# Kernel optimization log

Measured on AMD Instinct MI355X. Metric: run time of the kernel, lower is better.

Reference implementation:

```python
import math
import jax, jax.numpy as jnp
import numpy as np

B, N, C, H = 64, 197, 768, 12
KEEP_RATE = 0.7

def setup_inputs() -> dict:
    key = jax.random.key(0)
    k0, k1, k2 = jax.random.split(key, 3)
    x = jax.random.normal(k0, (B, N, C), jnp.float32)
    qkv_w = jax.random.normal(k1, (C, 3 * C), jnp.float32) * 0.02
    qkv_b = jnp.zeros((3 * C,), jnp.float32)
    proj_w = jax.random.normal(k2, (C, C), jnp.float32) * 0.02
    proj_b = jnp.zeros((C,), jnp.float32)
    return {"x": x, "qkv_w": qkv_w, "qkv_b": qkv_b, "proj_w": proj_w, "proj_b": proj_b}

def reference(x, qkv_w, qkv_b, proj_w, proj_b):
    b, n, c = x.shape
    d = c // H
    scale = d ** -0.5
    # qkv: [B,N,3C] -> [3,B,H,N,d]
    qkv = (x @ qkv_w + qkv_b).reshape(b, n, 3, H, d)
    qkv = jnp.transpose(qkv, (2, 0, 3, 1, 4))
    q, k, v = qkv[0], qkv[1], qkv[2]
    attn = jax.nn.softmax(jnp.einsum('bhnd,bhmd->bhnm', q, k) * scale, axis=-1)  # [B,H,N,N]
    out = jnp.einsum('bhnm,bhmd->bhnd', attn, v)          # [B,H,N,d]
    out = jnp.transpose(out, (0, 2, 1, 3)).reshape(b, n, c)
    x_out = out @ proj_w + proj_b                          # [B,N,C]
    # dynamic token pruning via CLS attention (row 0, excluding CLS itself)
    left_tokens = math.ceil(KEEP_RATE * (n - 1))
    cls_attn = attn[:, :, 0, 1:].mean(axis=1)              # [B,N-1]
    _, idx = jax.lax.top_k(cls_attn, left_tokens)          # descending, sorted
    index = jnp.broadcast_to(idx[:, :, None], (b, left_tokens, c))
    return (x_out, index, idx, cls_attn, left_tokens)
```

## Files before the change

kernel.cpp:

```cpp
#include <hip/hip_runtime.h>
#include <math.h>

#define BB   64
#define NTOK 197
#define CC   768
#define HH   12
#define DH   64
#define MTOT (BB * NTOK)
#define MPAD 12672
#define LEFT 138

#define XOUT_OFF  0
#define INDEX_OFF 9682944
#define IDX_OFF   16465920
#define CLS_OFF   16474752
#define LT_OFF    16487296

typedef short s8v __attribute__((ext_vector_type(8)));
typedef short s4v __attribute__((ext_vector_type(4)));
typedef float f4v __attribute__((ext_vector_type(4)));

#define GLOAD16(g, l) __builtin_amdgcn_global_load_lds( \
    (const __attribute__((address_space(1))) unsigned int*)(g), \
    (__attribute__((address_space(3))) unsigned int*)(l), 16, 0, 0)

__device__ __forceinline__ unsigned short f2bf(float f) {
    union { float f; unsigned int i; } x; x.f = f;
    unsigned int r = x.i + 0x7FFFu + ((x.i >> 16) & 1u);
    return (unsigned short)(r >> 16);
}


__device__ __forceinline__ void convert_x_body(int blk, int tid,
        const float* __restrict__ in, unsigned short* __restrict__ outb)
{
    size_t i = ((size_t)blk * 256 + tid) * 8;
    float4 a = *(const float4*)(in + i);
    float4 b = *(const float4*)(in + i + 4);
    s8v r;
    r[0] = (short)f2bf(a.x); r[1] = (short)f2bf(a.y);
    r[2] = (short)f2bf(a.z); r[3] = (short)f2bf(a.w);
    r[4] = (short)f2bf(b.x); r[5] = (short)f2bf(b.y);
    r[6] = (short)f2bf(b.z); r[7] = (short)f2bf(b.w);
    *(s8v*)(outb + i) = r;
}

__device__ __forceinline__ void transpose_w_body(int q, int tid, char* smem,
        const float* __restrict__ inq, const float* __restrict__ inp,
        unsigned short* __restrict__ outq, unsigned short* __restrict__ outp)
{
    float (*tile)[33] = (float(*)[33])smem;
    const int bi = q % 24;
    int bj = q / 24;
    const float* in; unsigned short* outb; int N;
    if (bj < 72) { in = inq; outb = outq; N = 2304; }
    else         { bj -= 72; in = inp; outb = outp; N = 768; }
    const int tx = tid & 31, ty = tid >> 5;
#pragma unroll
    for (int r = ty; r < 32; r += 8)
        tile[r][tx] = in[(size_t)(bi * 32 + r) * N + bj * 32 + tx];
    __syncthreads();
#pragma unroll
    for (int r = ty; r < 32; r += 8)
        outb[(size_t)(bj * 32 + r) * 768 + bi * 32 + tx] = f2bf(tile[tx][r]);
}

#define QCH 64
__device__ __forceinline__ void qr_body(int blk, int tid, char* smem,
        const float* __restrict__ x, const float* __restrict__ qkv_w,
        const float* __restrict__ qkv_b, float* __restrict__ rws,
        float* __restrict__ bconst)
{
    const int b = blk / HH, h = blk - b * HH;
    float* x0    = (float*)smem;
    float* q0h   = (float*)(smem + 3072);
    float* wbuf0 = (float*)(smem + 3328);
    float* wbuf1 = (float*)(smem + 19712);
    for (int c = tid; c < CC; c += 256) x0[c] = x[(size_t)b * NTOK * CC + c];
    for (int u = tid; u < QCH * DH; u += 256) {
        int cc = u >> 6, o = u & 63;
        wbuf0[u] = qkv_w[(size_t)cc * 2304 + h * DH + o];
    }
    __syncthreads();
    float acc = 0.f;
    if (tid < DH) acc = qkv_b[h * DH + tid];
    for (int k = 0; k < CC / QCH; ++k) {
        float* wcur  = (k & 1) ? wbuf1 : wbuf0;
        float* wnext = (k & 1) ? wbuf0 : wbuf1;
        if (k + 1 < CC / QCH) {
            const int cbase = (k + 1) * QCH;
            for (int u = tid; u < QCH * DH; u += 256) {
                int cc = u >> 6, o = u & 63;
                wnext[u] = qkv_w[(size_t)(cbase + cc) * 2304 + h * DH + o];
            }
        }
        if (tid < DH) {
            const int cbase = k * QCH;
#pragma unroll
            for (int cc = 0; cc < QCH; ++cc)
                acc = fmaf(x0[cbase + cc], wcur[cc * 64 + tid], acc);
        }
        __syncthreads();
    }
    if (tid < DH) q0h[tid] = acc;
    __syncthreads();
    for (int c = tid; c < CC; c += 256) {
        const float* wrow = qkv_w + (size_t)c * 2304 + CC + h * DH;
        float acc2 = 0.f;
#pragma unroll
        for (int d = 0; d < DH; d += 4) {
            float4 w4 = *(const float4*)(wrow + d);
            acc2 = fmaf(w4.x, q0h[d + 0], acc2);
            acc2 = fmaf(w4.y, q0h[d + 1], acc2);
            acc2 = fmaf(w4.z, q0h[d + 2], acc2);
            acc2 = fmaf(w4.w, q0h[d + 3], acc2);
        }
        rws[((size_t)b * HH + h) * CC + c] = acc2;
    }
    if (tid == 0) {
        float acc3 = 0.f;
        for (int d = 0; d < DH; ++d) acc3 += q0h[d] * qkv_b[CC + h * DH + d];
        bconst[blk] = acc3;
    }
}

__device__ __forceinline__ void gemm_body(int id, int tid, char* smem,
        const unsigned short* __restrict__ A, const unsigned short* __restrict__ BT,
        const float* __restrict__ bias, int ncolt, int mode,
        unsigned short* __restrict__ outb, float* __restrict__ outf)
{
    const int xcd = id & 7;
    const int t = id >> 3;
    const int ct = t % ncolt, s = t / ncolt;
    const int rt = s * 8 + xcd;
    if (rt >= 99) return;
    const int m0 = rt * 128, n0 = ct * 128;

    const int wave = tid >> 6, lane = tid & 63;
    const int quad = lane >> 4, l16 = lane & 15;
    const int rowbase = (wave >> 1) * 64, colbase = (wave & 1) * 64;
    short* As = (short*)smem;
    short* Bs = (short*)(smem + 16384);

    const int rA   = lane >> 3;
    const int gcol = ((lane & 7) ^ rA) * 8;
    unsigned int agof[4], bgof[4];
#pragma unroll
    for (int i = 0; i < 4; ++i) {
        int c = wave * 4 + i;
        agof[i] = (unsigned int)((m0 + c * 8 + rA) * 768 + gcol);
        bgof[i] = (unsigned int)((n0 + c * 8 + rA) * 768 + gcol);
    }
    int aoff[4], boff[4];
#pragma unroll
    for (int i = 0; i < 4; ++i) {
        aoff[i] = (rowbase + i * 16 + l16) * 64 + ((quad ^ (l16 & 7)) * 8);
        boff[i] = (colbase + i * 16 + l16) * 64 + ((quad ^ (l16 & 7)) * 8);
    }

    f4v acc[4][4];
#pragma unroll
    for (int i = 0; i < 4; ++i)
#pragma unroll
        for (int j = 0; j < 4; ++j) acc[i][j] = (f4v)0.f;

    for (int k0 = 0; k0 < 768; k0 += 64) {
#pragma unroll
        for (int i = 0; i < 4; ++i) {
            int c = wave * 4 + i;
            GLOAD16(A  + agof[i] + k0, &As[c * 512]);
            GLOAD16(BT + bgof[i] + k0, &Bs[c * 512]);
        }
        __syncthreads();
#pragma unroll
        for (int ks = 0; ks < 2; ++ks) {
            const int x = ks * 32;
            s8v af[4], bf[4];
#pragma unroll
            for (int i = 0; i < 4; ++i) af[i] = *(const s8v*)&As[aoff[i] ^ x];
#pragma unroll
            for (int j = 0; j < 4; ++j) bf[j] = *(const s8v*)&Bs[boff[j] ^ x];
#pragma unroll
            for (int i = 0; i < 4; ++i)
#pragma unroll
                for (int j = 0; j < 4; ++j)
                    acc[i][j] = __builtin_amdgcn_mfma_f32_16x16x32_bf16(bf[j], af[i], acc[i][j], 0, 0, 0);
        }
        __syncthreads();
    }

    const int ncols = mode ? 768 : 2304;
#pragma unroll
    for (int i = 0; i < 4; ++i) {
        const int m = m0 + rowbase + i * 16 + l16;
        if (m >= MTOT) continue;
#pragma unroll
        for (int j = 0; j < 4; ++j) {
            const int nb = n0 + colbase + j * 16 + quad * 4;
            float4 b4 = *(const float4*)&bias[nb];
            if (mode == 1) {
                float4 r;
                r.x = acc[i][j][0] + b4.x; r.y = acc[i][j][1] + b4.y;
                r.z = acc[i][j][2] + b4.z; r.w = acc[i][j][3] + b4.w;
                *(float4*)(outf + (size_t)m * ncols + nb) = r;
            } else {
                s4v r;
                r[0] = (short)f2bf(acc[i][j][0] + b4.x);
                r[1] = (short)f2bf(acc[i][j][1] + b4.y);
                r[2] = (short)f2bf(acc[i][j][2] + b4.z);
                r[3] = (short)f2bf(acc[i][j][3] + b4.w);
                *(s4v*)(outb + (size_t)m * ncols + nb) = r;
            }
        }
    }
}

__device__ __forceinline__ void cls_s_body(int q, int tid, char* smem,
        const float* __restrict__ x, const float* __restrict__ rws,
        const float* __restrict__ bconst, float* __restrict__ sws)
{
    const int bx = q % 10, b = q / 10;
    float* rl  = (float*)smem;
    float* bcs = (float*)(smem + 37056);
#pragma unroll
    for (int h = 0; h < HH; ++h)
        for (int c = tid; c < CC; c += 256)
            rl[h * 772 + c] = rws[((size_t)b * HH + h) * CC + c];
    if (tid < HH) bcs[tid] = bconst[b * HH + tid];
    __syncthreads();
    const int local = bx * 256 + tid;
    if (local < NTOK * HH) {
        const int tok = local / HH;
        const int h = local - tok * HH;
        const float* xr = x + ((size_t)b * NTOK + tok) * CC;
        const float* rp = rl + h * 772;
        float acc = 0.f;
#pragma unroll 8
        for (int c = 0; c < CC; c += 4) {
            float4 x4 = *(const float4*)(xr + c);
            float4 r4 = *(const float4*)(rp + c);
            acc = fmaf(x4.x, r4.x, acc);
            acc = fmaf(x4.y, r4.y, acc);
            acc = fmaf(x4.z, r4.z, acc);
            acc = fmaf(x4.w, r4.w, acc);
        }
        sws[((size_t)b * HH + h) * NTOK + tok] = (acc + bcs[h]) * 0.125f;
    }
}

#define VTS 224
__device__ __forceinline__ void transpose_v_body(int q, int tid, char* smem,
        const unsigned short* __restrict__ qkv, unsigned short* __restrict__ vt)
{
    short (*tile)[33] = (short(*)[33])smem;
    const int bx = q % 7;
    const int by = (q / 7) & 1;
    const int bh = q / 14;
    const int b = bh / HH, h = bh - b * HH;
    const int tx = tid & 31, ty = tid >> 5;
    const unsigned short* vin = qkv + (size_t)b * NTOK * 2304 + 1536 + h * DH;
#pragma unroll
    for (int r = ty; r < 32; r += 8) {
        const int tok = bx * 32 + r;
        tile[r][tx] = (tok < NTOK) ? (short)vin[(size_t)tok * 2304 + by * 32 + tx] : (short)0;
    }
    __syncthreads();
#pragma unroll
    for (int r = ty; r < 32; r += 8) {
        const int d = by * 32 + r;
        vt[((size_t)bh * DH + d) * VTS + bx * 32 + tx] = tile[tx][r];
    }
}

__device__ __forceinline__ void cls_topk_body(int b, int tid, char* smem,
        const float* __restrict__ sws, float* __restrict__ out, int write_lt)
{
    const int wave = tid >> 6, lane = tid & 63;
    float (*sbuf)[208] = (float(*)[208])smem;
    float (*pm)[208]   = (float(*)[208])(smem + 9984);
    float* vals        = (float*)(smem + 13312);
    int*   idxs        = (int*)(smem + 14336);

    for (int jj = lane; jj < 208; jj += 64) pm[wave][jj] = 0.f;
    if (tid < NTOK) {
#pragma unroll
        for (int h = 0; h < HH; ++h)
            sbuf[h][tid] = sws[((size_t)b * HH + h) * NTOK + tid];
    }
    __syncthreads();

    for (int h = wave; h < HH; h += 4) {
        float sv[4], ev[4];
        float mx = -1e30f;
#pragma unroll
        for (int t = 0; t < 4; ++t) {
            int j = lane + 64 * t;
            sv[t] = (j < NTOK) ? sbuf[h][j] : -1e30f;
            mx = fmaxf(mx, sv[t]);
        }
#pragma unroll
        for (int off = 1; off < 64; off <<= 1) mx = fmaxf(mx, __shfl_xor(mx, off, 64));
        float sm = 0.f;
#pragma unroll
        for (int t = 0; t < 4; ++t) {
            int j = lane + 64 * t;
            ev[t] = (j < NTOK) ? expf(sv[t] - mx) : 0.f;
            sm += ev[t];
        }
#pragma unroll
        for (int off = 1; off < 64; off <<= 1) sm += __shfl_xor(sm, off, 64);
#pragma unroll
        for (int t = 0; t < 4; ++t) {
            int j = lane + 64 * t;
            if (j < NTOK) pm[wave][j] += ev[t] / sm;
        }
    }
    __syncthreads();

    float v = -INFINITY;
    int id = 256 + tid;
    if (tid < NTOK - 1) {
        int j = tid + 1;
        float s = ((pm[0][j] + pm[1][j]) + (pm[2][j] + pm[3][j])) * (1.f / 12.f);
        v = s; id = tid;
        out[CLS_OFF + (size_t)b * (NTOK - 1) + tid] = s;
    }
    vals[tid] = v; idxs[tid] = id;
    __syncthreads();

    for (int k = 2; k <= 256; k <<= 1) {
        for (int j = k >> 1; j > 0; j >>= 1) {
            int ixj = tid ^ j;
            if (ixj > tid) {
                float va = vals[tid], vb2 = vals[ixj];
                int ia = idxs[tid], ib = idxs[ixj];
                bool aLess = (va > vb2) || (va == vb2 && ia < ib);
                bool dir = ((tid & k) == 0);
                if (dir != aLess) {
                    vals[tid] = vb2; vals[ixj] = va;
                    idxs[tid] = ib;  idxs[ixj] = ia;
                }
            }
            __syncthreads();
        }
    }

    if (tid < LEFT) out[IDX_OFF + (size_t)b * LEFT + tid] = (float)idxs[tid];
    if (write_lt && b == 0 && tid == 0) out[LT_OFF] = (float)LEFT;
}

__device__ __forceinline__ void write_index_body(int row, int tid,
        const float* __restrict__ idx_in, float* __restrict__ out)
{
    const float v = idx_in[row];
    if (tid < 192) {
        float4 r; r.x = v; r.y = v; r.z = v; r.w = v;
        *(float4*)(out + INDEX_OFF + (size_t)row * CC + tid * 4) = r;
    }
}

#define PRE_QR 768
#define PRE_CV 4728
#define PRE_TW 2304

__global__ __launch_bounds__(256)
void fat_pre(const float* __restrict__ x, const float* __restrict__ qkv_w,
             const float* __restrict__ qkv_b, const float* __restrict__ proj_w,
             unsigned short* __restrict__ xbf, unsigned short* __restrict__ wt1,
             unsigned short* __restrict__ wt2, float* __restrict__ rws,
             float* __restrict__ bconst)
{
    __shared__ __align__(16) char smem[36096];
    const int id = blockIdx.x, tid = threadIdx.x;
    if (id < PRE_QR)
        qr_body(id, tid, smem, x, qkv_w, qkv_b, rws, bconst);
    else if (id < PRE_QR + PRE_CV)
        convert_x_body(id - PRE_QR, tid, x, xbf);
    else
        transpose_w_body(id - PRE_QR - PRE_CV, tid, smem, qkv_w, proj_w, wt1, wt2);
}

#define QKV_GEMM (8 * 18 * 13)

__global__ __launch_bounds__(256, 3)
void fat_qkv(const unsigned short* __restrict__ xbf, const unsigned short* __restrict__ wt1,
             const float* __restrict__ qkv_b, unsigned short* __restrict__ qkvbf,
             const float* __restrict__ x, const float* __restrict__ rws,
             const float* __restrict__ bconst, float* __restrict__ sws)
{
    __shared__ __align__(16) char smem[37104];
    const int id = blockIdx.x, tid = threadIdx.x;
    if (id < QKV_GEMM)
        gemm_body(id, tid, smem, xbf, wt1, qkv_b, 18, 0, qkvbf, nullptr);
    else
        cls_s_body(id - QKV_GEMM, tid, smem, x, rws, bconst, sws);
}

__global__ __launch_bounds__(256)
void fat_tv(const unsigned short* __restrict__ qkvbf, unsigned short* __restrict__ vt,
            const float* __restrict__ sws, float* __restrict__ out, int write_lt)
{
    __shared__ __align__(16) char smem[15360];
    const int id = blockIdx.x, tid = threadIdx.x;
    if (id < 64)
        cls_topk_body(id, tid, smem, sws, out, write_lt);
    else
        transpose_v_body(id - 64, tid, smem, qkvbf, vt);
}

#define PROJ_GEMM (8 * 6 * 13)

__global__ __launch_bounds__(256, 3)
void fat_proj(const unsigned short* __restrict__ atbf, const unsigned short* __restrict__ wt2,
              const float* __restrict__ proj_b, float* __restrict__ outf,
              const float* __restrict__ idx_in, float* __restrict__ out)
{
    __shared__ __align__(16) char smem[32768];
    const int id = blockIdx.x, tid = threadIdx.x;
    if (id < PROJ_GEMM)
        gemm_body(id, tid, smem, atbf, wt2, proj_b, 6, 1, nullptr, outf);
    else
        write_index_body(id - PROJ_GEMM, tid, idx_in, out);
}

#define PSTR 226

__global__ __launch_bounds__(256, 2)
void attn_mfma4(const unsigned short* __restrict__ qkv, const unsigned short* __restrict__ vt,
                unsigned short* __restrict__ attnbf)
{
    const int bh = blockIdx.x;
    const int g  = blockIdx.y;
    const int b = bh / HH, h = bh - b * HH;
    const int tid = threadIdx.x;
    const int wave = tid >> 6, lane = tid & 63;
    const int quad = lane >> 4, l16 = lane & 15;
    __shared__ __align__(16) short Ks[NTOK * 64];
    __shared__ short Ps[4][16 * PSTR];

    const unsigned short* qg = qkv + (size_t)b * NTOK * 2304 + h * DH;
    const unsigned short* kg = qg + 768;
    const unsigned short* vtb = vt + (size_t)bh * DH * VTS;

    for (int u = tid; u < NTOK * 8; u += 256) {
        const int row = u >> 3, seg = u & 7;
        *(s8v*)&Ks[row * 64 + (seg ^ (row & 7)) * 8] =
            *(const s8v*)(kg + (size_t)row * 2304 + seg * 8);
    }
    __syncthreads();

    const int strip = g * 4 + wave;
    if (strip >= 13) return;

    const int mq = min(strip * 16 + l16, NTOK - 1);
    const s8v aq0 = *(const s8v*)(qg + (size_t)mq * 2304 + quad * 8);
    const s8v aq1 = *(const s8v*)(qg + (size_t)mq * 2304 + 32 + quad * 8);

    f4v sacc[14];
#pragma unroll
    for (int j = 0; j < 14; ++j) sacc[j] = (f4v)0.f;
    __builtin_amdgcn_s_setprio(1);
#pragma unroll
    for (int j = 0; j < 14; ++j) {
        const int kt = min(j * 16 + l16, NTOK - 1);
        s8v bk0 = *(const s8v*)&Ks[kt * 64 + ((quad       ^ (kt & 7)) * 8)];
        s8v bk1 = *(const s8v*)&Ks[kt * 64 + (((quad + 4) ^ (kt & 7)) * 8)];
        sacc[j] = __builtin_amdgcn_mfma_f32_16x16x32_bf16(bk0, aq0, sacc[j], 0, 0, 0);
        sacc[j] = __builtin_amdgcn_mfma_f32_16x16x32_bf16(bk1, aq1, sacc[j], 0, 0, 0);
    }
    __builtin_amdgcn_s_setprio(0);

    s8v bvr[7][4];
#pragma unroll
    for (int t = 0; t < 7; ++t) {
        const int ko = t * 32 + quad * 8;
#pragma unroll
        for (int j = 0; j < 4; ++j)
            bvr[t][j] = *(const s8v*)(vtb + (size_t)(j * 16 + l16) * VTS + ko);
    }

    float mx = -1e30f;
#pragma unroll
    for (int j = 0; j < 14; ++j)
#pragma unroll
        for (int r = 0; r < 4; ++r) {
            const int key = j * 16 + quad * 4 + r;
            float s = (key < NTOK) ? sacc[j][r] * 0.125f : -1e30f;
            sacc[j][r] = s;
            mx = fmaxf(mx, s);
        }
    mx = fmaxf(mx, __shfl_xor(mx, 16, 64));
    mx = fmaxf(mx, __shfl_xor(mx, 32, 64));

    float sm = 0.f;
#pragma unroll
    for (int j = 0; j < 14; ++j) {
        s4v pk;
#pragma unroll
        for (int r = 0; r < 4; ++r) {
            const int key = j * 16 + quad * 4 + r;
            float p = (key < NTOK) ? __expf(sacc[j][r] - mx) : 0.f;
            sm += p;
            pk[r] = (short)f2bf(p);
        }
        *(s4v*)&Ps[wave][l16 * PSTR + j * 16 + quad * 4] = pk;
    }
    sm += __shfl_xor(sm, 16, 64);
    sm += __shfl_xor(sm, 32, 64);
    const float rcp = 1.f / sm;

    f4v oacc[4];
#pragma unroll
    for (int j = 0; j < 4; ++j) oacc[j] = (f4v)0.f;
    __builtin_amdgcn_s_setprio(1);
#pragma unroll
    for (int t = 0; t < 7; ++t) {
        const int ko = t * 32 + quad * 8;
        s8v ap = *(const s8v*)&Ps[wave][l16 * PSTR + ko];
#pragma unroll
        for (int j = 0; j < 4; ++j)
            oacc[j] = __builtin_amdgcn_mfma_f32_16x16x32_bf16(bvr[t][j], ap, oacc[j], 0, 0, 0);
    }
    __builtin_amdgcn_s_setprio(0);
    const int qrow = strip * 16 + l16;
    if (qrow < NTOK) {
#pragma unroll
        for (int j = 0; j < 4; ++j) {
            s4v o4;
#pragma unroll
            for (int r = 0; r < 4; ++r) o4[r] = (short)f2bf(oacc[j][r] * rcp);
            *(s4v*)&attnbf[((size_t)b * NTOK + qrow) * 768 + h * DH + j * 16 + quad * 4] = o4;
        }
    }
}

extern "C" void kernel_launch(void* const* d_in, const int* in_sizes, int n_in,
                              void* d_out, int out_size, void* d_ws, size_t ws_size,
                              hipStream_t stream)
{
    const float* x      = (const float*)d_in[0];
    const float* qkv_w  = (const float*)d_in[1];
    const float* qkv_b  = (const float*)d_in[2];
    const float* proj_w = (const float*)d_in[3];
    const float* proj_b = (const float*)d_in[4];
    float* out = (float*)d_out;

    char* w = (char*)d_ws;
    unsigned short* xbf   = (unsigned short*)w; w += (size_t)MPAD * CC * 2;
    unsigned short* wt1   = (unsigned short*)w; w += (size_t)3 * CC * CC * 2;
    unsigned short* wt2   = (unsigned short*)w; w += (size_t)CC * CC * 2;
    unsigned short* qkvbf = (unsigned short*)w; w += (size_t)MTOT * 3 * CC * 2;
    unsigned short* atbf  = (unsigned short*)w; w += (size_t)MPAD * CC * 2;
    float* rws    = (float*)w; w += (size_t)BB * HH * CC * 4;
    float* bconst = (float*)w; w += (size_t)BB * HH * 4;
    float* sws    = (float*)w; w += (size_t)BB * HH * NTOK * 4;
    unsigned short* vtbf  = (unsigned short*)d_ws;

    fat_pre<<<dim3(PRE_QR + PRE_CV + PRE_TW), 256, 0, stream>>>(
        x, qkv_w, qkv_b, proj_w, xbf, wt1, wt2, rws, bconst);
    fat_qkv<<<dim3(QKV_GEMM + 640), 256, 0, stream>>>(
        xbf, wt1, qkv_b, qkvbf, x, rws, bconst, sws);
    fat_tv<<<dim3(64 + 7 * 2 * BB * HH), 256, 0, stream>>>(
        qkvbf, vtbf, sws, out, (out_size > LT_OFF) ? 1 : 0);
    attn_mfma4<<<dim3(BB * HH, 4), 256, 0, stream>>>(qkvbf, vtbf, atbf);
    fat_proj<<<dim3(PROJ_GEMM + BB * LEFT), 256, 0, stream>>>(
        atbf, wt2, proj_b, out + XOUT_OFF, out + IDX_OFF, out);
}
```

Baseline: 311.1 us.

## Batch CLS query projection over 8 batches per block; move index writes into attention kernel

The CLS-query projection now runs in 96 blocks, each covering 8 batch elements for one head instead of one (batch, head) pair. Each qkv_w slice is then loaded once and reused across 8 batches, and all 256 threads do work rather than 64. The broadcast index output writes move from the projection GEMM launch into the attention launch, so the proj GEMM runs alone. The trade-off is larger shared memory per fat_pre block (about 58 KB), which may reduce how many blocks fit per CU.

Measured after the change: 334.6 us. +7.6%, slower.

```diff
diff --git a/kernel.cpp b/kernel.cpp
--- a/kernel.cpp
+++ b/kernel.cpp
@@ -65,62 +65,83 @@
         outb[(size_t)(bj * 32 + r) * 768 + bi * 32 + tx] = f2bf(tile[tx][r]);
 }
 
-#define QCH 64
-__device__ __forceinline__ void qr_body(int blk, int tid, char* smem,
+#define QCH  64
+#define BGRP 8
+__device__ __forceinline__ void qr96_body(int q, int tid, char* smem,
         const float* __restrict__ x, const float* __restrict__ qkv_w,
         const float* __restrict__ qkv_b, float* __restrict__ rws,
         float* __restrict__ bconst)
 {
-    const int b = blk / HH, h = blk - b * HH;
-    float* x0    = (float*)smem;
-    float* q0h   = (float*)(smem + 3072);
-    float* wbuf0 = (float*)(smem + 3328);
-    float* wbuf1 = (float*)(smem + 19712);
-    for (int c = tid; c < CC; c += 256) x0[c] = x[(size_t)b * NTOK * CC + c];
+    const int h  = q % HH;
+    const int b0 = (q / HH) * BGRP;
+    float (*x0s)[CC] = (float(*)[CC])smem;
+    float* wbuf0 = (float*)(smem + 24576);
+    float* wbuf1 = (float*)(smem + 40960);
+    float (*q0s)[DH] = (float(*)[DH])(smem + 57344);
+
+    for (int u = tid; u < BGRP * CC; u += 256) {
+        int b = u / CC, c = u - b * CC;
+        x0s[b][c] = x[(size_t)(b0 + b) * NTOK * CC + c];
+    }
     for (int u = tid; u < QCH * DH; u += 256) {
-        int cc = u >> 6, o = u & 63;
-        wbuf0[u] = qkv_w[(size_t)cc * 2304 + h * DH + o];
-    }
-    __syncthreads();
-    float acc = 0.f;
-    if (tid < DH) acc = qkv_b[h * DH + tid];
+        int cc = u >> 6, dd = u & 63;
+        wbuf0[u] = qkv_w[(size_t)cc * 2304 + h * DH + dd];
+    }
+    __syncthreads();
+
+    const int d  = tid & 63;
+    const int bA = tid >> 6;
+    const int bB = bA + 4;
+    float accA = qkv_b[h * DH + d];
+    float accB = qkv_b[h * DH + d];
     for (int k = 0; k < CC / QCH; ++k) {
         float* wcur  = (k & 1) ? wbuf1 : wbuf0;
         float* wnext = (k & 1) ? wbuf0 : wbuf1;
         if (k + 1 < CC / QCH) {
             const int cbase = (k + 1) * QCH;
             for (int u = tid; u < QCH * DH; u += 256) {
-                int cc = u >> 6, o = u & 63;
-                wnext[u] = qkv_w[(size_t)(cbase + cc) * 2304 + h * DH + o];
+                int cc = u >> 6, dd = u & 63;
+                wnext[u] = qkv_w[(size_t)(cbase + cc) * 2304 + h * DH + dd];
             }
         }
-        if (tid < DH) {
-            const int cbase = k * QCH;
-#pragma unroll
-            for (int cc = 0; cc < QCH; ++cc)
-                acc = fmaf(x0[cbase + cc], wcur[cc * 64 + tid], acc);
+        const int cb = k * QCH;
+#pragma unroll
+        for (int cc = 0; cc < QCH; ++cc) {
+            const float wv = wcur[cc * 64 + d];
+            accA = fmaf(x0s[bA][cb + cc], wv, accA);
+            accB = fmaf(x0s[bB][cb + cc], wv, accB);
         }
         __syncthreads();
     }
-    if (tid < DH) q0h[tid] = acc;
-    __syncthreads();
+    q0s[bA][d] = accA;
+    q0s[bB][d] = accB;
+    __syncthreads();
+
+    if (tid < BGRP) {
+        float acc3 = 0.f;
+        for (int dd = 0; dd < DH; ++dd) acc3 += q0s[tid][dd] * qkv_b[CC + h * DH + dd];
+        bconst[(b0 + tid) * HH + h] = acc3;
+    }
+
     for (int c = tid; c < CC; c += 256) {
         const float* wrow = qkv_w + (size_t)c * 2304 + CC + h * DH;
-        float acc2 = 0.f;
-#pragma unroll
-        for (int d = 0; d < DH; d += 4) {
-            float4 w4 = *(const float4*)(wrow + d);
-            acc2 = fmaf(w4.x, q0h[d + 0], acc2);
-            acc2 = fmaf(w4.y, q0h[d + 1], acc2);
-            acc2 = fmaf(w4.z, q0h[d + 2], acc2);
-            acc2 = fmaf(w4.w, q0h[d + 3], acc2);
-        }
-        rws[((size_t)b * HH + h) * CC + c] = acc2;
-    }
-    if (tid == 0) {
-        float acc3 = 0.f;
-        for (int d = 0; d < DH; ++d) acc3 += q0h[d] * qkv_b[CC + h * DH + d];
-        bconst[blk] = acc3;
+        float acc2[BGRP];
+#pragma unroll
+        for (int b = 0; b < BGRP; ++b) acc2[b] = 0.f;
+#pragma unroll
+        for (int dd = 0; dd < DH; dd += 4) {
+            float4 w4 = *(const float4*)(wrow + dd);
+#pragma unroll
+            for (int b = 0; b < BGRP; ++b) {
+                acc2[b] = fmaf(w4.x, q0s[b][dd + 0], acc2[b]);
+                acc2[b] = fmaf(w4.y, q0s[b][dd + 1], acc2[b]);
+                acc2[b] = fmaf(w4.z, q0s[b][dd + 2], acc2[b]);
+                acc2[b] = fmaf(w4.w, q0s[b][dd + 3], acc2[b]);
+            }
+        }
+#pragma unroll
+        for (int b = 0; b < BGRP; ++b)
+            rws[((size_t)(b0 + b) * HH + h) * CC + c] = acc2[b];
     }
 }
 
@@ -359,7 +380,113 @@
     }
 }
 
-#define PRE_QR 768
+#define PSTR 226
+__device__ __forceinline__ void attn_body(int bh, int g, int tid,
+        short* Ks, short* Ps,
+        const unsigned short* __restrict__ qkv, const unsigned short* __restrict__ vt,
+        unsigned short* __restrict__ attnbf)
+{
+    const int b = bh / HH, h = bh - b * HH;
+    const int wave = tid >> 6, lane = tid & 63;
+    const int quad = lane >> 4, l16 = lane & 15;
+
+    const unsigned short* qg = qkv + (size_t)b * NTOK * 2304 + h * DH;
+    const unsigned short* kg = qg + 768;
+    const unsigned short* vtb = vt + (size_t)bh * DH * VTS;
+
+    for (int u = tid; u < NTOK * 8; u += 256) {
+        const int row = u >> 3, seg = u & 7;
+        *(s8v*)&Ks[row * 64 + (seg ^ (row & 7)) * 8] =
+            *(const s8v*)(kg + (size_t)row * 2304 + seg * 8);
+    }
+    __syncthreads();
+
+    const int strip = g * 4 + wave;
+    if (strip >= 13) return;
+
+    const int mq = min(strip * 16 + l16, NTOK - 1);
+    const s8v aq0 = *(const s8v*)(qg + (size_t)mq * 2304 + quad * 8);
+    const s8v aq1 = *(const s8v*)(qg + (size_t)mq * 2304 + 32 + quad * 8);
+
+    f4v sacc[14];
+#pragma unroll
+    for (int j = 0; j < 14; ++j) sacc[j] = (f4v)0.f;
+    __builtin_amdgcn_s_setprio(1);
+#pragma unroll
+    for (int j = 0; j < 14; ++j) {
+        const int kt = min(j * 16 + l16, NTOK - 1);
+        s8v bk0 = *(const s8v*)&Ks[kt * 64 + ((quad       ^ (kt & 7)) * 8)];
+        s8v bk1 = *(const s8v*)&Ks[kt * 64 + (((quad + 4) ^ (kt & 7)) * 8)];
+        sacc[j] = __builtin_amdgcn_mfma_f32_16x16x32_bf16(bk0, aq0, sacc[j], 0, 0, 0);
+        sacc[j] = __builtin_amdgcn_mfma_f32_16x16x32_bf16(bk1, aq1, sacc[j], 0, 0, 0);
+    }
+    __builtin_amdgcn_s_setprio(0);
+
+    s8v bvr[7][4];
+#pragma unroll
+    for (int t = 0; t < 7; ++t) {
+        const int ko = t * 32 + quad * 8;
+#pragma unroll
+        for (int j = 0; j < 4; ++j)
+            bvr[t][j] = *(const s8v*)(vtb + (size_t)(j * 16 + l16) * VTS + ko);
+    }
+
+    float mx = -1e30f;
+#pragma unroll
+    for (int j = 0; j < 14; ++j)
+#pragma unroll
+        for (int r = 0; r < 4; ++r) {
+            const int key = j * 16 + quad * 4 + r;
+            float s = (key < NTOK) ? sacc[j][r] * 0.125f : -1e30f;
+            sacc[j][r] = s;
+            mx = fmaxf(mx, s);
+        }
+    mx = fmaxf(mx, __shfl_xor(mx, 16, 64));
+    mx = fmaxf(mx, __shfl_xor(mx, 32, 64));
+
+    float sm = 0.f;
+#pragma unroll
+    for (int j = 0; j < 14; ++j) {
+        s4v pk;
+#pragma unroll
+        for (int r = 0; r < 4; ++r) {
+            const int key = j * 16 + quad * 4 + r;
+            float p = (key < NTOK) ? __expf(sacc[j][r] - mx) : 0.f;
+            sm += p;
+            pk[r] = (short)f2bf(p);
+        }
+        *(s4v*)&Ps[wave * 16 * PSTR + l16 * PSTR + j * 16 + quad * 4] = pk;
+    }
+    sm += __shfl_xor(sm, 16, 64);
+    sm += __shfl_xor(sm, 32, 64);
+    const float rcp = 1.f / sm;
+
+    f4v oacc[4];
+#pragma unroll
+    for (int j = 0; j < 4; ++j) oacc[j] = (f4v)0.f;
+    __builtin_amdgcn_s_setprio(1);
+#pragma unroll
+    for (int t = 0; t < 7; ++t) {
+        const int ko = t * 32 + quad * 8;
+        s8v ap = *(const s8v*)&Ps[wave * 16 * PSTR + l16 * PSTR + ko];
+#pragma unroll
+        for (int j = 0; j < 4; ++j)
+            oacc[j] = __builtin_amdgcn_mfma_f32_16x16x32_bf16(bvr[t][j], ap, oacc[j], 0, 0, 0);
+    }
+    __builtin_amdgcn_s_setprio(0);
+    const int qrow = strip * 16 + l16;
+    if (qrow < NTOK) {
+#pragma unroll
+        for (int j = 0; j < 4; ++j) {
+            s4v o4;
+#pragma unroll
+            for (int r = 0; r < 4; ++r) o4[r] = (short)f2bf(oacc[j][r] * rcp);
+            *(s4v*)&attnbf[((size_t)b * NTOK + qrow) * 768 + h * DH + j * 16 + quad * 4] = o4;
+        }
+    }
+}
+
+#define PRE_QR 96
 #define PRE_CV 4728
 #define PRE_TW 2304
 
@@ -370,10 +497,10 @@
              unsigned short* __restrict__ wt2, float* __restrict__ rws,
              float* __restrict__ bconst)
 {
-    __shared__ __align__(16) char smem[36096];
+    __shared__ __align__(16) char smem[59392];
     const int id = blockIdx.x, tid = threadIdx.x;
     if (id < PRE_QR)
-        qr_body(id, tid, smem, x, qkv_w, qkv_b, rws, bconst);
+        qr96_body(id, tid, smem, x, qkv_w, qkv_b, rws, bconst);
     else if (id < PRE_QR + PRE_CV)
         convert_x_body(id - PRE_QR, tid, x, xbf);
     else
@@ -408,130 +535,30 @@
         transpose_v_body(id - 64, tid, smem, qkvbf, vt);
 }
 
+#define ATTN_BLKS (768 * 4)
+
+__global__ __launch_bounds__(256, 2)
+void fat_attn(const unsigned short* __restrict__ qkv, const unsigned short* __restrict__ vt,
+              unsigned short* __restrict__ attnbf,
+              const float* __restrict__ idx_in, float* __restrict__ out)
+{
+    __shared__ __align__(16) short Ks[NTOK * 64];
+    __shared__ short Ps[4 * 16 * PSTR];
+    const int id = blockIdx.x, tid = threadIdx.x;
+    if (id < ATTN_BLKS)
+        attn_body(id % 768, id / 768, tid, Ks, Ps, qkv, vt, attnbf);
+    else
+        write_index_body(id - ATTN_BLKS, tid, idx_in, out);
+}
+
 #define PROJ_GEMM (8 * 6 * 13)
 
 __global__ __launch_bounds__(256, 3)
 void fat_proj(const unsigned short* __restrict__ atbf, const unsigned short* __restrict__ wt2,
-              const float* __restrict__ proj_b, float* __restrict__ outf,
-              const float* __restrict__ idx_in, float* __restrict__ out)
+              const float* __restrict__ proj_b, float* __restrict__ outf)
 {
     __shared__ __align__(16) char smem[32768];
-    const int id = blockIdx.x, tid = threadIdx.x;
-    if (id < PROJ_GEMM)
-        gemm_body(id, tid, smem, atbf, wt2, proj_b, 6, 1, nullptr, outf);
-    else
-        write_index_body(id - PROJ_GEMM, tid, idx_in, out);
-}
-
-#define PSTR 226
-
-__global__ __launch_bounds__(256, 2)
-void attn_mfma4(const unsigned short* __restrict__ qkv, const unsigned short* __restrict__ vt,
-                unsigned short* __restrict__ attnbf)
-{
-    const int bh = blockIdx.x;
-    const int g  = blockIdx.y;
-    const int b = bh / HH, h = bh - b * HH;
-    const int tid = threadIdx.x;
-    const int wave = tid >> 6, lane = tid & 63;
-    const int quad = lane >> 4, l16 = lane & 15;
-    __shared__ __align__(16) short Ks[NTOK * 64];
-    __shared__ short Ps[4][16 * PSTR];
-
-    const unsigned short* qg = qkv + (size_t)b * NTOK * 2304 + h * DH;
-    const unsigned short* kg = qg + 768;
-    const unsigned short* vtb = vt + (size_t)bh * DH * VTS;
-
-    for (int u = tid; u < NTOK * 8; u += 256) {
-        const int row = u >> 3, seg = u & 7;
-        *(s8v*)&Ks[row * 64 + (seg ^ (row & 7)) * 8] =
-            *(const s8v*)(kg + (size_t)row * 2304 + seg * 8);
-    }
-    __syncthreads();
-
-    const int strip = g * 4 + wave;
-    if (strip >= 13) return;
-
-    const int mq = min(strip * 16 + l16, NTOK - 1);
-    const s8v aq0 = *(const s8v*)(qg + (size_t)mq * 2304 + quad * 8);
-    const s8v aq1 = *(const s8v*)(qg + (size_t)mq * 2304 + 32 + quad * 8);
-
-    f4v sacc[14];
-#pragma unroll
-    for (int j = 0; j < 14; ++j) sacc[j] = (f4v)0.f;
-    __builtin_amdgcn_s_setprio(1);
-#pragma unroll
-    for (int j = 0; j < 14; ++j) {
-        const int kt = min(j * 16 + l16, NTOK - 1);
-        s8v bk0 = *(const s8v*)&Ks[kt * 64 + ((quad       ^ (kt & 7)) * 8)];
-        s8v bk1 = *(const s8v*)&Ks[kt * 64 + (((quad + 4) ^ (kt & 7)) * 8)];
-        sacc[j] = __builtin_amdgcn_mfma_f32_16x16x32_bf16(bk0, aq0, sacc[j], 0, 0, 0);
-        sacc[j] = __builtin_amdgcn_mfma_f32_16x16x32_bf16(bk1, aq1, sacc[j], 0, 0, 0);
-    }
-    __builtin_amdgcn_s_setprio(0);
-
-    s8v bvr[7][4];
-#pragma unroll
-    for (int t = 0; t < 7; ++t) {
-        const int ko = t * 32 + quad * 8;
-#pragma unroll
-        for (int j = 0; j < 4; ++j)
-            bvr[t][j] = *(const s8v*)(vtb + (size_t)(j * 16 + l16) * VTS + ko);
-    }
-
-    float mx = -1e30f;
-#pragma unroll
-    for (int j = 0; j < 14; ++j)
-#pragma unroll
-        for (int r = 0; r < 4; ++r) {
-            const int key = j * 16 + quad * 4 + r;
-            float s = (key < NTOK) ? sacc[j][r] * 0.125f : -1e30f;
-            sacc[j][r] = s;
-            mx = fmaxf(mx, s);
-        }
-    mx = fmaxf(mx, __shfl_xor(mx, 16, 64));
-    mx = fmaxf(mx, __shfl_xor(mx, 32, 64));
-
-    float sm = 0.f;
-#pragma unroll
-    for (int j = 0; j < 14; ++j) {
-        s4v pk;
-#pragma unroll
-        for (int r = 0; r < 4; ++r) {
-            const int key = j * 16 + quad * 4 + r;
-            float p = (key < NTOK) ? __expf(sacc[j][r] - mx) : 0.f;
-            sm += p;
-            pk[r] = (short)f2bf(p);
-        }
-        *(s4v*)&Ps[wave][l16 * PSTR + j * 16 + quad * 4] = pk;
-    }
-    sm += __shfl_xor(sm, 16, 64);
-    sm += __shfl_xor(sm, 32, 64);
-    const float rcp = 1.f / sm;
-
-    f4v oacc[4];
-#pragma unroll
-    for (int j = 0; j < 4; ++j) oacc[j] = (f4v)0.f;
-    __builtin_amdgcn_s_setprio(1);
-#pragma unroll
-    for (int t = 0; t < 7; ++t) {
-        const int ko = t * 32 + quad * 8;
-        s8v ap = *(const s8v*)&Ps[wave][l16 * PSTR + ko];
-#pragma unroll
-        for (int j = 0; j < 4; ++j)
-            oacc[j] = __builtin_amdgcn_mfma_f32_16x16x32_bf16(bvr[t][j], ap, oacc[j], 0, 0, 0);
-    }
-    __builtin_amdgcn_s_setprio(0);
-    const int qrow = strip * 16 + l16;
-    if (qrow < NTOK) {
-#pragma unroll
-        for (int j = 0; j < 4; ++j) {
-            s4v o4;
-#pragma unroll
-            for (int r = 0; r < 4; ++r) o4[r] = (short)f2bf(oacc[j][r] * rcp);
-            *(s4v*)&attnbf[((size_t)b * NTOK + qrow) * 768 + h * DH + j * 16 + quad * 4] = o4;
-        }
-    }
+    gemm_body(blockIdx.x, threadIdx.x, smem, atbf, wt2, proj_b, 6, 1, nullptr, outf);
 }
 
 extern "C" void kernel_launch(void* const* d_in, const int* in_sizes, int n_in,
@@ -562,7 +589,7 @@
         xbf, wt1, qkv_b, qkvbf, x, rws, bconst, sws);
     fat_tv<<<dim3(64 + 7 * 2 * BB * HH), 256, 0, stream>>>(
         qkvbf, vtbf, sws, out, (out_size > LT_OFF) ? 1 : 0);
-    attn_mfma4<<<dim3(BB * HH, 4), 256, 0, stream>>>(qkvbf, vtbf, atbf);
-    fat_proj<<<dim3(PROJ_GEMM + BB * LEFT), 256, 0, stream>>>(
-        atbf, wt2, proj_b, out + XOUT_OFF, out + IDX_OFF, out);
-}
+    fat_attn<<<dim3(ATTN_BLKS + BB * LEFT), 256, 0, stream>>>(
+        qkvbf, vtbf, atbf, out + IDX_OFF, out);
+    fat_proj<<<dim3(PROJ_GEMM), 256, 0, stream>>>(atbf, wt2, proj_b, out + XOUT_OFF);
+}
```
